# Optimization experiments

Hardware: AMD Instinct MI355X
Metric: run time of the kernel (lower is better)

Reference implementation:

```python
import jax, jax.numpy as jnp
import numpy as np
import math

D_MODEL = 256
D_STATE = 16
D_CONV = 4
EXPAND = 2
D_INNER = EXPAND * D_MODEL          # 512
DT_RANK = math.ceil(D_MODEL / 16)   # 16
EPS = 1e-5


def rmsnorm(x, w):
    return x * jax.lax.rsqrt(jnp.mean(x * x, axis=-1, keepdims=True) + EPS) * w


def mamba_mixer(x, in_proj, conv_w, conv_b, x_proj, dt_w, dt_b, A_log, Dp, out_proj):
    # x: [B, L, d_model]
    Bsz, L, _ = x.shape
    xz = x @ in_proj.T                       # [B, L, 2*d_inner]
    xh, z = jnp.split(xz, 2, axis=-1)        # each [B, L, d_inner]
    # causal depthwise conv1d over time (d_conv=4)
    xp = jnp.pad(xh, ((0, 0), (D_CONV - 1, 0), (0, 0)))
    xc = sum(xp[:, k:k + L, :] * conv_w[:, k] for k in range(D_CONV)) + conv_b
    xc = jax.nn.silu(xc)                     # [B, L, d_inner]
    x_dbl = xc @ x_proj.T                    # [B, L, dt_rank + 2*d_state]
    dt, Bm, Cm = jnp.split(x_dbl, [DT_RANK, DT_RANK + D_STATE], axis=-1)
    delta = jax.nn.softplus(dt @ dt_w.T + dt_b)   # [B, L, d_inner]
    A = -jnp.exp(A_log)                      # [d_inner, d_state]
    dA = jnp.exp(jnp.einsum('bld,dn->lbdn', delta, A))        # [L,B,d,n]
    dBu = jnp.einsum('bld,bln,bld->lbdn', delta, Bm, xc)       # [L,B,d,n]

    def step(h, inp):
        a, b = inp
        h = a * h + b
        return h, h

    h0 = jnp.zeros((Bsz, D_INNER, D_STATE), xc.dtype)
    _, hs = jax.lax.scan(step, h0, (dA, dBu))                  # [L,B,d,n]
    y = jnp.einsum('lbdn,bln->bld', hs, Cm) + xc * Dp          # [B,L,d_inner]
    y = y * jax.nn.silu(z)
    return y @ out_proj.T                                      # [B,L,d_model]


def block(x, norm_w, in_proj, conv_w, conv_b, x_proj, dt_w, dt_b, A_log, Dp, out_proj):
    # Block with fused_add_norm=False, residual=None: residual = x, h = mixer(norm(x))
    residual = x
    h = mamba_mixer(rmsnorm(x, norm_w), in_proj, conv_w, conv_b, x_proj,
                    dt_w, dt_b, A_log, Dp, out_proj)
    return h + residual


def setup_inputs() -> dict:
    key = jax.random.key(0)
    ks = jax.random.split(key, 16)
    B, L = 4, 2048

    def n(k, shape, s=0.02):
        return jax.random.normal(k, shape, jnp.float32) * s

    inp = {"x": jax.random.normal(ks[0], (B, L, D_MODEL), jnp.float32)}
    i = 1
    for pre in ("fw", "bw"):
        inp[pre + "_norm"] = jnp.ones((D_MODEL,), jnp.float32)
        inp[pre + "_in_proj"] = n(ks[i], (2 * D_INNER, D_MODEL)); i += 1
        inp[pre + "_conv_w"] = n(ks[i], (D_INNER, D_CONV), 0.1); i += 1
        inp[pre + "_conv_b"] = jnp.zeros((D_INNER,), jnp.float32)
        inp[pre + "_x_proj"] = n(ks[i], (DT_RANK + 2 * D_STATE, D_INNER)); i += 1
        inp[pre + "_dt_w"] = n(ks[i], (D_INNER, DT_RANK), 0.1); i += 1
        inp[pre + "_dt_b"] = n(ks[i], (D_INNER,), 0.1); i += 1
        inp[pre + "_A_log"] = jnp.log(jnp.tile(jnp.arange(1, D_STATE + 1, dtype=jnp.float32), (D_INNER, 1)))
        inp[pre + "_D"] = jnp.ones((D_INNER,), jnp.float32)
        inp[pre + "_out_proj"] = n(ks[i], (D_MODEL, D_INNER)); i += 1
    return inp


def reference(x,
              fw_norm, fw_in_proj, fw_conv_w, fw_conv_b, fw_x_proj, fw_dt_w, fw_dt_b, fw_A_log, fw_D, fw_out_proj,
              bw_norm, bw_in_proj, bw_conv_w, bw_conv_b, bw_x_proj, bw_dt_w, bw_dt_b, bw_A_log, bw_D, bw_out_proj):
    fwd = block(x, fw_norm, fw_in_proj, fw_conv_w, fw_conv_b, fw_x_proj,
                fw_dt_w, fw_dt_b, fw_A_log, fw_D, fw_out_proj)
    xb = jnp.flip(x, axis=1)
    bwd = block(xb, bw_norm, bw_in_proj, bw_conv_w, bw_conv_b, bw_x_proj,
                bw_dt_w, bw_dt_b, bw_A_log, bw_D, bw_out_proj)
    bwd = jnp.flip(bwd, axis=1)
    return fwd + bwd
```

## Files before the change

### kernel.cpp

```cpp
#include <hip/hip_runtime.h>
#include <hip/hip_bf16.h>
#include <math.h>


#define NTOK 8192
#define LL   2048
#define DM   256
#define DI   512
#define DS2  16
#define CL   64
#define NCH  32
#define PLANE 65536
#define KSTEP 64

typedef __bf16 bf16x8 __attribute__((ext_vector_type(8)));
typedef float f32x4 __attribute__((ext_vector_type(4)));

__device__ inline unsigned short f2bf(float f) {
    unsigned u = __float_as_uint(f);
    unsigned r = (u + 0x7fffu + ((u >> 16) & 1u)) >> 16;
    return (unsigned short)r;
}
__device__ inline float bf2f(unsigned short s) {
    return __uint_as_float((unsigned)s << 16);
}

#define L2E 1.4426950408889634f
#define LN2 0.6931471805599453f

__device__ inline float softplus_fast(float x) {
    float e = __builtin_amdgcn_exp2f(-fabsf(x) * L2E);
    float l = __builtin_amdgcn_logf(1.f + e);
    return fmaxf(x, 0.f) + l * LN2;
}

__device__ inline int xcd_swz(int bid, int nwg) {
    int q = nwg >> 3, r = nwg & 7;
    int xcd = bid & 7, lo = bid >> 3;
    return (xcd < r ? xcd * (q + 1) : r * (q + 1) + (xcd - r) * q) + lo;
}

#define GLDS(gp, lp) __builtin_amdgcn_global_load_lds( \
    (const __attribute__((address_space(1))) void*)(gp), \
    (__attribute__((address_space(3))) void*)(lp), 16, 0, 0)

__global__ __launch_bounds__(256) void prep_kernel(
    const float* __restrict__ ip0, const float* __restrict__ nw0,
    const float* __restrict__ ip1, const float* __restrict__ nw1,
    const float* __restrict__ xp0, const float* __restrict__ dtw0,
    const float* __restrict__ xp1, const float* __restrict__ dtw1,
    const float* __restrict__ op0, const float* __restrict__ op1,
    unsigned short* __restrict__ w_in, unsigned short* __restrict__ w_p2,
    unsigned short* __restrict__ w_out,
    const float* __restrict__ x, unsigned short* __restrict__ xn) {
    int bid = blockIdx.x, tid = threadIdx.x;
    if (bid < 2048) {
        int dir = bid >> 10, n = bid & 1023;
        const float* ip = dir ? ip1 : ip0;
        const float* nw = dir ? nw1 : nw0;
        w_in[(size_t)bid * 256 + tid] = f2bf(ip[n * 256 + tid] * nw[tid]);
    } else if (bid < 3200) {
        int idx = bid - 2048;
        int dir = idx / 576, row = idx % 576;
        const float* xp = dir ? xp1 : xp0;
        const float* dtw = dir ? dtw1 : dtw0;
        unsigned short* dst = w_p2 + (size_t)idx * 512;
        for (int k = tid; k < 512; k += 256) {
            float v = 0.f;
            if (row < 512) {
                #pragma unroll
                for (int r = 0; r < 16; ++r) v = fmaf(dtw[row * 16 + r], xp[r * 512 + k], v);
            } else if (row < 544) {
                v = xp[(16 + row - 512) * 512 + k];
            }
            dst[k] = f2bf(v);
        }
    } else if (bid < 3456) {
        int n = bid - 3200;
        for (int k = tid; k < 1024; k += 256) {
            float v = (k < 512) ? op0[n * 512 + k] : op1[n * 512 + (k - 512)];
            w_out[(size_t)n * 1024 + k] = f2bf(v);
        }
    } else {
        int t = bid - 3456;
        float v = x[(size_t)t * DM + tid];
        float ss = v * v;
        #pragma unroll
        for (int m = 1; m < 64; m <<= 1) ss += __shfl_xor(ss, m);
        __shared__ float ws[4];
        if ((tid & 63) == 0) ws[tid >> 6] = ss;
        __syncthreads();
        float tot = ws[0] + ws[1] + ws[2] + ws[3];
        float scale = rsqrtf(tot / (float)DM + 1e-5f);
        xn[(size_t)t * DM + tid] = f2bf(v * scale);
    }
}

#define EPI_IN  0
#define EPI_P2  1
#define EPI_OUT 2

template <int EPI>
__global__ __launch_bounds__(256) void mfma_gemm(
    const unsigned short* __restrict__ A0, const unsigned short* __restrict__ A1,
    const unsigned short* __restrict__ Wb, int K,
    unsigned short* __restrict__ d0, unsigned short* __restrict__ d1,
    unsigned short* __restrict__ e0, unsigned short* __restrict__ e1,
    const float* __restrict__ aux0, const float* __restrict__ aux1,
    const float* __restrict__ Xres, float* __restrict__ outF) {
    __shared__ char lds[2][2][8192];
    int tid = threadIdx.x;
    int lane = tid & 63, wid = tid >> 6;
    int wm = wid >> 1, wn = wid & 1;
    int nwg = gridDim.x * gridDim.y;
    int lid = xcd_swz(blockIdx.y * gridDim.x + blockIdx.x, nwg);
    int n0 = (lid % gridDim.x) * 64;
    int m0 = (lid / gridDim.x) * 64;
    int dir = blockIdx.z;
    const unsigned short* A = dir ? A1 : A0;
    const unsigned short* W = Wb + ((EPI == EPI_P2) ? (size_t)dir * 576 * 512 : 0);

    const int s1 = tid, s2 = tid + 256;
    const int r1 = s1 >> 3, c1 = (s1 & 7) ^ (r1 & 7);
    const int r2 = s2 >> 3, c2 = (s2 & 7) ^ (r2 & 7);

    f32x4 acc[2][2] = {};
    int nt = K / KSTEP;

    auto stage = [&](int t, int buf) {
        int k0 = t * KSTEP;
        GLDS(A + (size_t)(m0 + r1) * K + k0 + c1 * 8, &lds[buf][0][0] + wid * 1024);
        GLDS(A + (size_t)(m0 + r2) * K + k0 + c2 * 8, &lds[buf][0][0] + 4096 + wid * 1024);
        GLDS(W + (size_t)(n0 + r1) * K + k0 + c1 * 8, &lds[buf][1][0] + wid * 1024);
        GLDS(W + (size_t)(n0 + r2) * K + k0 + c2 * 8, &lds[buf][1][0] + 4096 + wid * 1024);
    };

    stage(0, 0);
    for (int t = 0; t < nt; ++t) {
        int buf = t & 1;
        __syncthreads();
        if (t + 1 < nt) stage(t + 1, buf ^ 1);
        const char* Ab = &lds[buf][0][0];
        const char* Bb = &lds[buf][1][0];
        bf16x8 af[2][2], bfv[2][2];
        #pragma unroll
        for (int mf = 0; mf < 2; ++mf)
            #pragma unroll
            for (int kf = 0; kf < 2; ++kf) {
                int r = wm * 32 + mf * 16 + (lane & 15);
                int c = (lane >> 4) + kf * 4;
                af[mf][kf] = *(const bf16x8*)(Ab + r * 128 + ((c ^ (r & 7)) << 4));
            }
        #pragma unroll
        for (int nf = 0; nf < 2; ++nf)
            #pragma unroll
            for (int kf = 0; kf < 2; ++kf) {
                int r = wn * 32 + nf * 16 + (lane & 15);
                int c = (lane >> 4) + kf * 4;
                bfv[nf][kf] = *(const bf16x8*)(Bb + r * 128 + ((c ^ (r & 7)) << 4));
            }
        #pragma unroll
        for (int kf = 0; kf < 2; ++kf)
            #pragma unroll
            for (int mf = 0; mf < 2; ++mf)
                #pragma unroll
                for (int nf = 0; nf < 2; ++nf)
                    acc[mf][nf] = __builtin_amdgcn_mfma_f32_16x16x32_bf16(
                        af[mf][kf], bfv[nf][kf], acc[mf][nf], 0, 0, 0);
    }

    int cb0 = n0 + wn * 32 + (lane & 15);
    int rb0 = m0 + wm * 32 + ((lane >> 4) << 2);
    #pragma unroll
    for (int mf = 0; mf < 2; ++mf)
        #pragma unroll
        for (int nf = 0; nf < 2; ++nf) {
            int n = cb0 + nf * 16;
            #pragma unroll
            for (int r = 0; r < 4; ++r) {
                int m = rb0 + mf * 16 + r;
                float v = acc[mf][nf][r];
                if (EPI == EPI_IN) {
                    d0[(size_t)m * 2048 + n] = f2bf(v);
                } else if (EPI == EPI_P2) {
                    if (n < 512) {
                        float sv = v + (dir ? aux1 : aux0)[n];
                        (dir ? d1 : d0)[(size_t)m * 512 + n] = f2bf(softplus_fast(sv));
                    } else if (n < 544) {
                        (dir ? e1 : e0)[(size_t)m * 32 + (n - 512)] = f2bf(v);
                    }
                } else {
                    outF[(size_t)m * 256 + n] = v + 2.f * Xres[(size_t)m * 256 + n];
                }
            }
        }
}

__global__ __launch_bounds__(256) void conv_silu_kernel(
    const unsigned short* __restrict__ xz,
    const float* __restrict__ cw0, const float* __restrict__ cw1,
    const float* __restrict__ cb0, const float* __restrict__ cb1,
    unsigned short* __restrict__ o0, unsigned short* __restrict__ o1) {
    int dir = blockIdx.y;
    const float* cw = dir ? cw1 : cw0;
    const float* cb = dir ? cb1 : cb0;
    unsigned short* xc = dir ? o1 : o0;
    int idx8 = blockIdx.x * 256 + threadIdx.x;
    int t = idx8 >> 6;
    int c8 = (idx8 & 63) << 3;
    int l = t & (LL - 1);
    const unsigned short* xh = xz + (size_t)dir * 1024 + c8;

    float wreg[32];
    #pragma unroll
    for (int q = 0; q < 8; ++q)
        *(float4*)&wreg[q * 4] = *(const float4*)&cw[c8 * 4 + q * 4];
    float acc[8];
    *(float4*)&acc[0] = *(const float4*)&cb[c8];
    *(float4*)&acc[4] = *(const float4*)&cb[c8 + 4];

    #pragma unroll
    for (int k = 0; k < 4; ++k) {
        int lo = dir ? (l + 3 - k) : (l - 3 + k);
        if (lo < 0 || lo >= LL) continue;
        uint4 u = *(const uint4*)(xh + (size_t)(t + lo - l) * 2048);
        unsigned wv[4] = {u.x, u.y, u.z, u.w};
        #pragma unroll
        for (int j = 0; j < 4; ++j) {
            float flo = __uint_as_float(wv[j] << 16);
            float fhi = __uint_as_float(wv[j] & 0xffff0000u);
            acc[2 * j]     = fmaf(flo, wreg[(2 * j) * 4 + k], acc[2 * j]);
            acc[2 * j + 1] = fmaf(fhi, wreg[(2 * j + 1) * 4 + k], acc[2 * j + 1]);
        }
    }
    unsigned out[4];
    #pragma unroll
    for (int j = 0; j < 4; ++j) {
        float a0 = acc[2 * j], a1 = acc[2 * j + 1];
        float s0 = a0 / (1.f + __expf(-a0));
        float s1 = a1 / (1.f + __expf(-a1));
        out[j] = (unsigned)f2bf(s0) | ((unsigned)f2bf(s1) << 16);
    }
    *(uint4*)(xc + (size_t)idx8 * 8) = make_uint4(out[0], out[1], out[2], out[3]);
}

__global__ __launch_bounds__(128, 2) void scan_part1(
    const unsigned short* __restrict__ dlt0, const unsigned short* __restrict__ dlt1,
    const unsigned short* __restrict__ xc0, const unsigned short* __restrict__ xc1,
    const unsigned short* __restrict__ bc0, const unsigned short* __restrict__ bc1,
    const float* __restrict__ Al0, const float* __restrict__ Al1,
    const float* __restrict__ Dp0, const float* __restrict__ Dp1,
    float* __restrict__ AC, float* __restrict__ HC,
    unsigned* __restrict__ yls0, unsigned* __restrict__ yls1) {
    int dir = blockIdx.z;
    const unsigned short* delta = dir ? dlt1 : dlt0;
    const unsigned short* xc    = dir ? xc1 : xc0;
    const unsigned short* bc    = dir ? bc1 : bc0;
    const float* Alog           = dir ? Al1 : Al0;
    const float* Dp             = dir ? Dp1 : Dp0;
    unsigned* yls               = dir ? yls1 : yls0;
    int b = blockIdx.y >> 5, ch = blockIdx.y & 31;
    int d0 = blockIdx.x * 128;
    int tid = threadIdx.x;
    int d = d0 + tid;

    __shared__ unsigned sdxu[CL][128];
    __shared__ float sB[CL][16];
    __shared__ float sC[CL][16];
    {
        int row = tid >> 1, q2 = tid & 1;
        int lr = ch * CL + row;
        int l = dir ? (LL - 1 - lr) : lr;
        size_t t = (size_t)b * LL + l;
        const uint4* dp = (const uint4*)(delta + t * DI + d0) + q2 * 8;
        const uint4* xp = (const uint4*)(xc + t * DI + d0) + q2 * 8;
        #pragma unroll
        for (int hh = 0; hh < 8; ++hh) {
            uint4 du = dp[hh], xu = xp[hh];
            unsigned dw[4] = {du.x, du.y, du.z, du.w};
            unsigned xw[4] = {xu.x, xu.y, xu.z, xu.w};
            #pragma unroll
            for (int j = 0; j < 4; ++j) {
                int col = q2 * 64 + hh * 8 + 2 * j;
                sdxu[row][col ^ row]       = (dw[j] & 0xffffu) | (xw[j] << 16);
                sdxu[row][(col + 1) ^ row] = (dw[j] >> 16) | (xw[j] & 0xffff0000u);
            }
        }
        uint4 Bu = *(const uint4*)(bc + t * 32 + q2 * 8);
        uint4 Cu = *(const uint4*)(bc + t * 32 + 16 + q2 * 8);
        unsigned bw[4] = {Bu.x, Bu.y, Bu.z, Bu.w};
        unsigned cw[4] = {Cu.x, Cu.y, Cu.z, Cu.w};
        #pragma unroll
        for (int j = 0; j < 4; ++j) {
            sB[row][q2 * 8 + 2 * j]     = __uint_as_float(bw[j] << 16);
            sB[row][q2 * 8 + 2 * j + 1] = __uint_as_float(bw[j] & 0xffff0000u);
            sC[row][q2 * 8 + 2 * j]     = __uint_as_float(cw[j] << 16);
            sC[row][q2 * 8 + 2 * j + 1] = __uint_as_float(cw[j] & 0xffff0000u);
        }
    }
    __syncthreads();

    float Av[16], Avl[16];
    #pragma unroll
    for (int qq = 0; qq < 4; ++qq) {
        float4 Al = *(const float4*)&Alog[d * DS2 + qq * 4];
        Av[qq * 4 + 0] = -__expf(Al.x);
        Av[qq * 4 + 1] = -__expf(Al.y);
        Av[qq * 4 + 2] = -__expf(Al.z);
        Av[qq * 4 + 3] = -__expf(Al.w);
    }
    #pragma unroll
    for (int j = 0; j < 16; ++j) Avl[j] = Av[j] * L2E;
    bool fast = true;
    #pragma unroll
    for (int j = 0; j < 15; ++j)
        fast = fast && (fabsf(Av[j + 1] - Av[j] + 1.f) < 1e-2f);

    float Dv = Dp[d];
    float h[16];
    #pragma unroll
    for (int j = 0; j < 16; ++j) h[j] = 0.f;
    float sdl = 0.f;
    const float nL2E = -L2E;

    if (fast) {
        for (int r = 0; r < CL; ++r) {
            unsigned u = sdxu[r][tid ^ r];
            float dl = __uint_as_float(u << 16);
            float xcv = __uint_as_float(u & 0xffff0000u);
            float Bv[16], Cv[16];
            #pragma unroll
            for (int k = 0; k < 4; ++k) {
                *(float4*)&Bv[k * 4] = *(const float4*)&sB[r][k * 4];
                *(float4*)&Cv[k * 4] = *(const float4*)&sC[r][k * 4];
            }
            float u0 = dl * xcv;
            sdl += dl;
            float e0 = __builtin_amdgcn_exp2f(dl * Avl[0]);
            float rr = __builtin_amdgcn_exp2f(dl * nL2E);
            float rr2 = rr * rr, rr4 = rr2 * rr2, rr8 = rr4 * rr4;
            float e[16];
            e[0] = e0;       e[1] = e0 * rr;
            e[2] = e0 * rr2; e[3] = e[1] * rr2;
            #pragma unroll
            for (int j = 0; j < 4; ++j) e[4 + j] = e[j] * rr4;
            #pragma unroll
            for (int j = 0; j < 8; ++j) e[8 + j] = e[j] * rr8;
            float t0 = 0.f, t1 = 0.f, t2 = 0.f, t3 = 0.f;
            #pragma unroll
            for (int j = 0; j < 4; ++j) {
                h[4*j+0] = fmaf(e[4*j+0], h[4*j+0], u0 * Bv[4*j+0]);
                h[4*j+1] = fmaf(e[4*j+1], h[4*j+1], u0 * Bv[4*j+1]);
                h[4*j+2] = fmaf(e[4*j+2], h[4*j+2], u0 * Bv[4*j+2]);
                h[4*j+3] = fmaf(e[4*j+3], h[4*j+3], u0 * Bv[4*j+3]);
                t0 = fmaf(h[4*j+0], Cv[4*j+0], t0);
                t1 = fmaf(h[4*j+1], Cv[4*j+1], t1);
                t2 = fmaf(h[4*j+2], Cv[4*j+2], t2);
                t3 = fmaf(h[4*j+3], Cv[4*j+3], t3);
            }
            float ts = (t0 + t1) + (t2 + t3);
            int lr = ch * CL + r;
            float yv = fmaf(xcv, Dv, ts);
            yls[((size_t)b * LL + lr) * DI + d] =
                (unsigned)f2bf(yv) | ((unsigned)f2bf(sdl) << 16);
        }
    } else {
        for (int r = 0; r < CL; ++r) {
            unsigned u = sdxu[r][tid ^ r];
            float dl = __uint_as_float(u << 16);
            float xcv = __uint_as_float(u & 0xffff0000u);
            float u0 = dl * xcv;
            sdl += dl;
            float ts = 0.f;
            #pragma unroll
            for (int j = 0; j < 16; ++j) {
                float e = __builtin_amdgcn_exp2f(dl * Avl[j]);
                h[j] = fmaf(e, h[j], u0 * sB[r][j]);
                ts = fmaf(h[j], sC[r][j], ts);
            }
            int lr = ch * CL + r;
            float yv = fmaf(xcv, Dv, ts);
            yls[((size_t)b * LL + lr) * DI + d] =
                (unsigned)f2bf(yv) | ((unsigned)f2bf(sdl) << 16);
        }
    }

    size_t base = (size_t)ch * PLANE + (size_t)(((dir * 4 + b) * DI + d) * DS2);
    float ac[16];
    #pragma unroll
    for (int j = 0; j < 16; ++j) ac[j] = __builtin_amdgcn_exp2f(Avl[j] * sdl);
    #pragma unroll
    for (int k = 0; k < 4; ++k) {
        *(float4*)&AC[base + k * 4] = *(const float4*)&ac[k * 4];
        *(float4*)&HC[base + k * 4] = *(const float4*)&h[k * 4];
    }
}

__global__ __launch_bounds__(256) void scan_part2(
    const float* __restrict__ AC, const float* __restrict__ HC,
    float* __restrict__ HIN) {
    int idx = blockIdx.x * 256 + threadIdx.x;
    float hin = 0.f;
    #pragma unroll
    for (int ch = 0; ch < NCH; ++ch) {
        size_t o = (size_t)ch * PLANE + idx;
        HIN[o] = hin;
        hin = fmaf(AC[o], hin, HC[o]);
    }
}

__global__ __launch_bounds__(256, 8) void scan_lite(
    const unsigned* __restrict__ yls0, const unsigned* __restrict__ yls1,
    const unsigned short* __restrict__ bc0, const unsigned short* __restrict__ bc1,
    const unsigned short* __restrict__ xz,
    const float* __restrict__ Al0, const float* __restrict__ Al1,
    const float* __restrict__ HIN, unsigned short* __restrict__ ycat) {
    int dir = blockIdx.z;
    const unsigned* yls         = dir ? yls1 : yls0;
    const unsigned short* bc    = dir ? bc1 : bc0;
    const float* Alog           = dir ? Al1 : Al0;
    int b = blockIdx.y >> 5, ch = blockIdx.y & 31;
    int d0 = blockIdx.x * 64;
    int tid = threadIdx.x;
    int dg = tid & 63, lg = tid >> 6;
    int d = d0 + dg;

    __shared__ unsigned sC[CL][8];
    {
        int row = tid >> 2, q = tid & 3;
        if (q < 2) {
            int lr = ch * CL + row;
            int l = dir ? (LL - 1 - lr) : lr;
            size_t t = (size_t)b * LL + l;
            uint4 cu = *(const uint4*)(bc + t * 32 + 16 + q * 8);
            *(uint4*)&sC[row][q * 4] = cu;
        }
    }
    __syncthreads();

    float Av[16];
    bool fastA = true;
    #pragma unroll
    for (int qq = 0; qq < 4; ++qq) {
        float4 Al = *(const float4*)&Alog[d * DS2 + qq * 4];
        Av[qq * 4 + 0] = -__expf(Al.x);
        Av[qq * 4 + 1] = -__expf(Al.y);
        Av[qq * 4 + 2] = -__expf(Al.z);
        Av[qq * 4 + 3] = -__expf(Al.w);
    }
    #pragma unroll
    for (int n = 0; n < 16; ++n)
        fastA = fastA && (fabsf(Av[n] + (float)(n + 1)) < 1e-3f * (float)(n + 1));

    float hin[16];
    size_t hbase = (size_t)ch * PLANE + (size_t)(((dir * 4 + b) * DI + d) * DS2);
    #pragma unroll
    for (int qq = 0; qq < 4; ++qq)
        *(float4*)&hin[qq * 4] = *(const float4*)&HIN[hbase + qq * 4];

    #pragma unroll 2
    for (int i = 0; i < 16; ++i) {
        int row = lg * 16 + i;
        int lr = ch * CL + row;
        int ll = dir ? (LL - 1 - lr) : lr;
        size_t tt = (size_t)b * LL + ll;
        unsigned u = yls[((size_t)b * LL + lr) * DI + d];
        float yv = __uint_as_float(u << 16);
        float s  = __uint_as_float(u & 0xffff0000u);
        if (fastA) {
            float E = __builtin_amdgcn_exp2f(-s * L2E);
            if (__any(E > 3e-6f)) {
                float acc = 0.f;
                #pragma unroll
                for (int p = 7; p >= 0; --p) {
                    unsigned cp = sC[row][p];
                    float C0 = __uint_as_float(cp << 16);
                    float C1 = __uint_as_float(cp & 0xffff0000u);
                    acc = fmaf(acc, E, C1 * hin[2 * p + 1]);
                    acc = fmaf(acc, E, C0 * hin[2 * p]);
                }
                yv = fmaf(acc, E, yv);
            }
        } else {
            float acc = 0.f;
            #pragma unroll
            for (int p = 0; p < 8; ++p) {
                unsigned cp = sC[row][p];
                float C0 = __uint_as_float(cp << 16);
                float C1 = __uint_as_float(cp & 0xffff0000u);
                float e0 = __builtin_amdgcn_exp2f(s * Av[2 * p] * L2E);
                float e1 = __builtin_amdgcn_exp2f(s * Av[2 * p + 1] * L2E);
                acc = fmaf(e0 * hin[2 * p], C0, acc);
                acc = fmaf(e1 * hin[2 * p + 1], C1, acc);
            }
            yv += acc;
        }
        float zz = bf2f(xz[tt * 2048 + (size_t)dir * 1024 + 512 + d]);
        yv *= zz / (1.f + __expf(-zz));
        ycat[tt * 1024 + (size_t)dir * 512 + d] = f2bf(yv);
    }
}

extern "C" void kernel_launch(void* const* d_in, const int* in_sizes, int n_in,
                              void* d_out, int out_size, void* d_ws, size_t ws_size,
                              hipStream_t stream) {
    const float* x = (const float*)d_in[0];
    const float* p[2][10];
    for (int dir = 0; dir < 2; ++dir)
        for (int i = 0; i < 10; ++i)
            p[dir][i] = (const float*)d_in[1 + dir * 10 + i];

    char* w = (char*)d_ws;
    auto alloc = [&](size_t bytes) { char* q = w; w += (bytes + 255) & ~(size_t)255; return q; };
    unsigned short* xn    = (unsigned short*)alloc((size_t)NTOK * DM * 2);
    unsigned short* w_in  = (unsigned short*)alloc((size_t)2048 * 256 * 2);
    unsigned short* w_p2  = (unsigned short*)alloc((size_t)1152 * 512 * 2);
    unsigned short* w_out = (unsigned short*)alloc((size_t)256 * 1024 * 2);
    unsigned short* xzcat = (unsigned short*)alloc((size_t)NTOK * 2048 * 2);
    unsigned short *xcb[2], *dlt[2], *bc[2];
    unsigned* yls[2];
    for (int dir = 0; dir < 2; ++dir) {
        xcb[dir] = (unsigned short*)alloc((size_t)NTOK * DI * 2);
        dlt[dir] = (unsigned short*)alloc((size_t)NTOK * DI * 2);
        bc[dir]  = (unsigned short*)alloc((size_t)NTOK * 32 * 2);
        yls[dir] = (unsigned*)alloc((size_t)NTOK * DI * 4);
    }
    unsigned short* ycat = (unsigned short*)alloc((size_t)NTOK * 1024 * 2);
    float* AC  = (float*)alloc((size_t)NCH * PLANE * 4);
    float* HC  = (float*)alloc((size_t)NCH * PLANE * 4);
    float* HIN = (float*)alloc((size_t)NCH * PLANE * 4);
    float* out = (float*)d_out;

    prep_kernel<<<3456 + NTOK, 256, 0, stream>>>(
        p[0][1], p[0][0], p[1][1], p[1][0],
        p[0][4], p[0][5], p[1][4], p[1][5],
        p[0][9], p[1][9], w_in, w_p2, w_out, x, xn);

    mfma_gemm<EPI_IN><<<dim3(32, 128, 1), 256, 0, stream>>>(
        xn, xn, w_in, 256, xzcat, nullptr, nullptr, nullptr,
        nullptr, nullptr, nullptr, nullptr);

    conv_silu_kernel<<<dim3(2048, 2), 256, 0, stream>>>(
        xzcat, p[0][2], p[1][2], p[0][3], p[1][3], xcb[0], xcb[1]);

    mfma_gemm<EPI_P2><<<dim3(9, 128, 2), 256, 0, stream>>>(
        xcb[0], xcb[1], w_p2, 512, dlt[0], dlt[1], bc[0], bc[1],
        p[0][6], p[1][6], nullptr, nullptr);

    scan_part1<<<dim3(DI / 128, 4 * NCH, 2), 128, 0, stream>>>(
        dlt[0], dlt[1], xcb[0], xcb[1], bc[0], bc[1], p[0][7], p[1][7],
        p[0][8], p[1][8], AC, HC, yls[0], yls[1]);
    scan_part2<<<PLANE / 256, 256, 0, stream>>>(AC, HC, HIN);
    scan_lite<<<dim3(DI / 64, 4 * NCH, 2), 256, 0, stream>>>(
        yls[0], yls[1], bc[0], bc[1], xzcat,
        p[0][7], p[1][7], HIN, ycat);

    mfma_gemm<EPI_OUT><<<dim3(4, 128, 1), 256, 0, stream>>>(
        ycat, ycat, w_out, 1024, nullptr, nullptr, nullptr, nullptr,
        nullptr, nullptr, x, out);
}
```

Before: 168.6 us.

## Make GEMM workgroups persistent over multiple M tiles with continuous prefetch

Each GEMM workgroup now walks several 64-row M tiles in sequence (8, 4 and 2 tiles for the three GEMMs). The double-buffered LDS prefetch keeps running across tile boundaries, and the epilogue is written inside the loop. K is made a compile-time template parameter. The aim is to cut launch and prologue cost per tile and hide the pipeline fill at each tile start. In exchange there are far fewer workgroups, which may underfill the CUs, and the epilogue stores now sit inside the main loop.

```diff
diff --git a/kernel.cpp b/kernel.cpp
--- a/kernel.cpp
+++ b/kernel.cpp
@@ -100,10 +100,10 @@
 #define EPI_P2  1
 #define EPI_OUT 2
 
-template <int EPI>
+template <int EPI, int K, int MLOOP>
 __global__ __launch_bounds__(256) void mfma_gemm(
     const unsigned short* __restrict__ A0, const unsigned short* __restrict__ A1,
-    const unsigned short* __restrict__ Wb, int K,
+    const unsigned short* __restrict__ Wb,
     unsigned short* __restrict__ d0, unsigned short* __restrict__ d1,
     unsigned short* __restrict__ e0, unsigned short* __restrict__ e1,
     const float* __restrict__ aux0, const float* __restrict__ aux1,
@@ -115,7 +115,7 @@
     int nwg = gridDim.x * gridDim.y;
     int lid = xcd_swz(blockIdx.y * gridDim.x + blockIdx.x, nwg);
     int n0 = (lid % gridDim.x) * 64;
-    int m0 = (lid / gridDim.x) * 64;
+    int mbase = (lid / gridDim.x) * (MLOOP * 64);
     int dir = blockIdx.z;
     const unsigned short* A = dir ? A1 : A0;
     const unsigned short* W = Wb + ((EPI == EPI_P2) ? (size_t)dir * 576 * 512 : 0);
@@ -124,10 +124,14 @@
     const int r1 = s1 >> 3, c1 = (s1 & 7) ^ (r1 & 7);
     const int r2 = s2 >> 3, c2 = (s2 & 7) ^ (r2 & 7);
 
+    constexpr int nt = K / KSTEP;
+    constexpr int total = MLOOP * nt;
+
     f32x4 acc[2][2] = {};
-    int nt = K / KSTEP;
-
-    auto stage = [&](int t, int buf) {
+
+    auto stage = [&](int it, int buf) {
+        int mi = it / nt, t = it % nt;
+        int m0 = mbase + mi * 64;
         int k0 = t * KSTEP;
         GLDS(A + (size_t)(m0 + r1) * K + k0 + c1 * 8, &lds[buf][0][0] + wid * 1024);
         GLDS(A + (size_t)(m0 + r2) * K + k0 + c2 * 8, &lds[buf][0][0] + 4096 + wid * 1024);
@@ -136,10 +140,10 @@
     };
 
     stage(0, 0);
-    for (int t = 0; t < nt; ++t) {
-        int buf = t & 1;
+    for (int it = 0; it < total; ++it) {
+        int buf = it & 1;
         __syncthreads();
-        if (t + 1 < nt) stage(t + 1, buf ^ 1);
+        if (it + 1 < total) stage(it + 1, buf ^ 1);
         const char* Ab = &lds[buf][0][0];
         const char* Bb = &lds[buf][1][0];
         bf16x8 af[2][2], bfv[2][2];
@@ -167,33 +171,42 @@
                 for (int nf = 0; nf < 2; ++nf)
                     acc[mf][nf] = __builtin_amdgcn_mfma_f32_16x16x32_bf16(
                         af[mf][kf], bfv[nf][kf], acc[mf][nf], 0, 0, 0);
-    }
-
-    int cb0 = n0 + wn * 32 + (lane & 15);
-    int rb0 = m0 + wm * 32 + ((lane >> 4) << 2);
-    #pragma unroll
-    for (int mf = 0; mf < 2; ++mf)
-        #pragma unroll
-        for (int nf = 0; nf < 2; ++nf) {
-            int n = cb0 + nf * 16;
-            #pragma unroll
-            for (int r = 0; r < 4; ++r) {
-                int m = rb0 + mf * 16 + r;
-                float v = acc[mf][nf][r];
-                if (EPI == EPI_IN) {
-                    d0[(size_t)m * 2048 + n] = f2bf(v);
-                } else if (EPI == EPI_P2) {
-                    if (n < 512) {
-                        float sv = v + (dir ? aux1 : aux0)[n];
-                        (dir ? d1 : d0)[(size_t)m * 512 + n] = f2bf(softplus_fast(sv));
-                    } else if (n < 544) {
-                        (dir ? e1 : e0)[(size_t)m * 32 + (n - 512)] = f2bf(v);
+
+        if ((it % nt) == nt - 1) {
+            int m0 = mbase + (it / nt) * 64;
+            int cb0 = n0 + wn * 32 + (lane & 15);
+            int rb0 = m0 + wm * 32 + ((lane >> 4) << 2);
+            #pragma unroll
+            for (int mf = 0; mf < 2; ++mf)
+                #pragma unroll
+                for (int nf = 0; nf < 2; ++nf) {
+                    int n = cb0 + nf * 16;
+                    #pragma unroll
+                    for (int r = 0; r < 4; ++r) {
+                        int m = rb0 + mf * 16 + r;
+                        float v = acc[mf][nf][r];
+                        if (EPI == EPI_IN) {
+                            d0[(size_t)m * 2048 + n] = f2bf(v);
+                        } else if (EPI == EPI_P2) {
+                            if (n < 512) {
+                                float sv = v + (dir ? aux1 : aux0)[n];
+                                (dir ? d1 : d0)[(size_t)m * 512 + n] = f2bf(softplus_fast(sv));
+                            } else if (n < 544) {
+                                (dir ? e1 : e0)[(size_t)m * 32 + (n - 512)] = f2bf(v);
+                            }
+                        } else {
+                            outF[(size_t)m * 256 + n] = v + 2.f * Xres[(size_t)m * 256 + n];
+                        }
                     }
-                } else {
-                    outF[(size_t)m * 256 + n] = v + 2.f * Xres[(size_t)m * 256 + n];
                 }
-            }
-        }
+            f32x4 z4 = {0.f, 0.f, 0.f, 0.f};
+            #pragma unroll
+            for (int mf = 0; mf < 2; ++mf)
+                #pragma unroll
+                for (int nf = 0; nf < 2; ++nf)
+                    acc[mf][nf] = z4;
+        }
+    }
 }
 
 __global__ __launch_bounds__(256) void conv_silu_kernel(
@@ -536,15 +549,15 @@
         p[0][4], p[0][5], p[1][4], p[1][5],
         p[0][9], p[1][9], w_in, w_p2, w_out, x, xn);
 
-    mfma_gemm<EPI_IN><<<dim3(32, 128, 1), 256, 0, stream>>>(
-        xn, xn, w_in, 256, xzcat, nullptr, nullptr, nullptr,
+    mfma_gemm<EPI_IN, 256, 8><<<dim3(32, 16, 1), 256, 0, stream>>>(
+        xn, xn, w_in, xzcat, nullptr, nullptr, nullptr,
         nullptr, nullptr, nullptr, nullptr);
 
     conv_silu_kernel<<<dim3(2048, 2), 256, 0, stream>>>(
         xzcat, p[0][2], p[1][2], p[0][3], p[1][3], xcb[0], xcb[1]);
 
-    mfma_gemm<EPI_P2><<<dim3(9, 128, 2), 256, 0, stream>>>(
-        xcb[0], xcb[1], w_p2, 512, dlt[0], dlt[1], bc[0], bc[1],
+    mfma_gemm<EPI_P2, 512, 4><<<dim3(9, 32, 2), 256, 0, stream>>>(
+        xcb[0], xcb[1], w_p2, dlt[0], dlt[1], bc[0], bc[1],
         p[0][6], p[1][6], nullptr, nullptr);
 
     scan_part1<<<dim3(DI / 128, 4 * NCH, 2), 128, 0, stream>>>(
@@ -555,7 +568,7 @@
         yls[0], yls[1], bc[0], bc[1], xzcat,
         p[0][7], p[1][7], HIN, ycat);
 
-    mfma_gemm<EPI_OUT><<<dim3(4, 128, 1), 256, 0, stream>>>(
-        ycat, ycat, w_out, 1024, nullptr, nullptr, nullptr, nullptr,
+    mfma_gemm<EPI_OUT, 1024, 2><<<dim3(4, 64, 1), 256, 0, stream>>>(
+        ycat, ycat, w_out, nullptr, nullptr, nullptr, nullptr,
         nullptr, nullptr, x, out);
 }
```

Measured after the change: 181.1 us. 1.07x slower.
